# Optimization experiments

Hardware: AMD Instinct MI355X
Metric: run time of the kernel (lower is better)

The kernel has to match this reference:

```python
import jax, jax.numpy as jnp
import numpy as np

N_HEADS = 4
N_HIDDEN = 64  # out_features // n_heads
NEG_SLOPE = 0.2


def setup_inputs() -> dict:
    key = jax.random.key(0)
    k1, k2, k3, k4, k5 = jax.random.split(key, 5)
    B, N, F_IN, F_OUT = 1, 4096, 128, 256
    h = jax.random.normal(k1, (B, N, F_IN), dtype=jnp.float32)
    adj_mat = jax.random.uniform(k2, (N, N, 1), dtype=jnp.float32)
    W_proj = jax.random.normal(k3, (F_IN, N_HEADS * N_HIDDEN), dtype=jnp.float32) / np.sqrt(F_IN)
    W_proj_attn = jax.random.normal(k4, (F_IN, N_HEADS * N_HIDDEN // 2), dtype=jnp.float32) / np.sqrt(F_IN)
    w_attn = jax.random.normal(k5, (N_HIDDEN,), dtype=jnp.float32) / np.sqrt(N_HIDDEN)
    return {"h": h, "adj_mat": adj_mat, "W_proj": W_proj, "W_proj_attn": W_proj_attn, "w_attn": w_attn}


def reference(h, adj_mat, W_proj, W_proj_attn, w_attn):
    B, N, _ = h.shape
    H, D = N_HEADS, N_HIDDEN
    half = D // 2
    # value projection: (B, N, H, D)
    g = (h @ W_proj).reshape(B, N, H, D)
    # attention-feature projection: (B, N, H, D//2)
    ga = (h @ W_proj_attn).reshape(B, N, H, half)
    # attn(cat([ga_i, ga_j])) decomposes linearly: e_ij = <w_l, ga_i> + <w_r, ga_j>
    # (identical math to the torch repeat/cat/Linear, without the NxNxD tensor)
    el = jnp.einsum('bnhk,k->bnh', ga, w_attn[:half])   # dest node i term
    er = jnp.einsum('bnhk,k->bnh', ga, w_attn[half:])   # source node j term
    e = jax.nn.leaky_relu(el[:, :, None, :] + er[:, None, :, :], NEG_SLOPE)  # (B, N, N, H)
    mask = adj_mat >= 0.5  # (N, N, 1) broadcasts over (B, N, N, H)
    e = jnp.where(mask, e, -jnp.inf)
    a = jax.nn.softmax(e, axis=2)  # softmax over source nodes j
    # dropout is identity in eval mode
    out = jnp.einsum('bijh,bjhf->bihf', a, g)  # (B, N, H, D)
    return out.reshape(B, N, H * D)  # is_concat=True
```

## Files before the change

kernel.cpp:

```cpp
#include <hip/hip_runtime.h>
#include <hip/hip_bf16.h>

typedef __bf16 bf16_t;
typedef __bf16 bf16x4 __attribute__((ext_vector_type(4)));
typedef __bf16 bf16x8 __attribute__((ext_vector_type(8)));
typedef float floatx4 __attribute__((ext_vector_type(4)));

#define N_NODES 4096
#define F_IN 128
#define NUM_HEADS 4
#define D_HID 64
#define F_OUT 256
#define NEG_SLOPE 0.2f

__global__ __launch_bounds__(384) void proj_kernel(
    const float* __restrict__ hmat, const float* __restrict__ Wp,
    const float* __restrict__ Wa, const float* __restrict__ wattn,
    bf16_t* __restrict__ GB, float* __restrict__ el,
    float* __restrict__ E1r, float* __restrict__ E2r)
{
    __shared__ float hl[4][F_IN];
    const int t = threadIdx.x;
    const int j0 = blockIdx.x * 4;

    if (t < 128) {
        const int jl = t >> 5, m0 = (t & 31) * 4;
        *reinterpret_cast<float4*>(&hl[jl][m0]) =
            *reinterpret_cast<const float4*>(&hmat[(size_t)(j0 + jl) * F_IN + m0]);
    }
    __syncthreads();

    float acc[4] = {0.f, 0.f, 0.f, 0.f};

    const float* wptr;
    int stride;
    if (t < 256) { wptr = Wp + t;         stride = 256; }
    else         { wptr = Wa + (t - 256); stride = 128; }

    for (int m = 0; m < F_IN; m += 4) {
        const float w0 = wptr[(size_t)(m + 0) * stride];
        const float w1 = wptr[(size_t)(m + 1) * stride];
        const float w2 = wptr[(size_t)(m + 2) * stride];
        const float w3 = wptr[(size_t)(m + 3) * stride];
#pragma unroll
        for (int jl = 0; jl < 4; ++jl) {
            const float4 hv = *reinterpret_cast<const float4*>(&hl[jl][m]);
            acc[jl] = fmaf(hv.w, w3, fmaf(hv.z, w2, fmaf(hv.y, w1, fmaf(hv.x, w0, acc[jl]))));
        }
    }

    if (t < 256) {
        const int h = t >> 6, f = t & 63;
        bf16x4 o;
#pragma unroll
        for (int q = 0; q < 4; ++q) o[q] = (bf16_t)acc[q];
        const size_t base = ((((size_t)h * 128 + (j0 >> 5)) * 4 + (f >> 4)) * 64
                             + (f & 15) + 16 * ((j0 >> 3) & 3)) * 8 + (j0 & 7);
        *reinterpret_cast<bf16x4*>(&GB[base]) = o;
    } else {
        const int ta = t - 256;
        const int ha = ta >> 5, k = ta & 31;
        const float wl = wattn[k], wr = wattn[32 + k];
#pragma unroll
        for (int jl = 0; jl < 4; ++jl) {
            float vl = acc[jl] * wl;
            float vr = acc[jl] * wr;
#pragma unroll
            for (int s = 16; s >= 1; s >>= 1) {
                vl += __shfl_xor(vl, s, 64);
                vr += __shfl_xor(vr, s, 64);
            }
            if (k == 0) {
                el[ha * N_NODES + j0 + jl]  = vl;
                E1r[ha * N_NODES + j0 + jl] = __expf(vr);
                E2r[ha * N_NODES + j0 + jl] = __expf(NEG_SLOPE * vr);
            }
        }
    }
}

__global__ __launch_bounds__(1024, 4) void attn_kernel(
    const float* __restrict__ adj, const bf16_t* __restrict__ GB,
    const float* __restrict__ el, const float* __restrict__ E1r,
    const float* __restrict__ E2r,
    float* __restrict__ numout, float* __restrict__ den_g,
    int njc, int ntiles)
{
    __shared__ bf16_t P_s[2][NUM_HEADS * 64 * 64];
    __shared__ bf16_t GB_s[2][32 * 512];

    const int tid = threadIdx.x;
    const int i0  = blockIdx.x * 64;
    const int jc  = blockIdx.y;
    const int jT0 = jc * ntiles * 64;

    const int pi   = tid >> 4;
    const int pj4  = (tid & 15) << 2;
    const int glog = pj4 >> 3;
    const int goff = pj4 & 7;
    const int psw  = ((glog ^ (pi & 7)) << 3) + goff;

    const int wave = tid >> 6;
    const int hh   = wave >> 2;
    const int mt   = wave & 3;
    const int lane = tid & 63;
    const int m    = lane & 15;
    const int quad = lane >> 4;

    float E1i[NUM_HEADS], E2i[NUM_HEADS], Ti[NUM_HEADS];
#pragma unroll
    for (int h = 0; h < NUM_HEADS; ++h) {
        const float e = el[h * N_NODES + i0 + pi];
        E1i[h] = __expf(e);
        E2i[h] = __expf(NEG_SLOPE * e);
        Ti[h]  = __expf(-e);
    }

    const float* adjp = adj + (size_t)(i0 + pi) * N_NODES + pj4;

    const int s0 = wave * 2, s1 = s0 + 1;
    const int s0h = (s0 >> 2) & 3, s0f = s0 & 3, s0j = s0 >> 4;
    const int s1h = (s1 >> 2) & 3, s1f = s1 & 3, s1j = s1 >> 4;

    floatx4 acc0 = {0.f, 0.f, 0.f, 0.f};
    floatx4 acc1 = acc0, acc2 = acc0, acc3 = acc0, accd = acc0;
    bf16x8 ones;
#pragma unroll
    for (int q = 0; q < 8; ++q) ones[q] = (bf16_t)1.0f;

    auto do_mfma = [&](int b) {
#pragma unroll
        for (int kt = 0; kt < 2; ++kt) {
            const int gphys = (((kt * 4 + quad) ^ (m & 7)) << 3);
            const bf16x8 af = *reinterpret_cast<const bf16x8*>(
                &P_s[b][(hh * 64 + mt * 16 + m) * 64 + gphys]);
            accd = __builtin_amdgcn_mfma_f32_16x16x32_bf16(af, ones, accd, 0, 0, 0);
            const int bb = (kt * 16 + hh * 4) * 512 + lane * 8;
            const bf16x8 b0 = *reinterpret_cast<const bf16x8*>(&GB_s[b][bb]);
            const bf16x8 b1 = *reinterpret_cast<const bf16x8*>(&GB_s[b][bb + 512]);
            const bf16x8 b2 = *reinterpret_cast<const bf16x8*>(&GB_s[b][bb + 1024]);
            const bf16x8 b3 = *reinterpret_cast<const bf16x8*>(&GB_s[b][bb + 1536]);
            acc0 = __builtin_amdgcn_mfma_f32_16x16x32_bf16(af, b0, acc0, 0, 0, 0);
            acc1 = __builtin_amdgcn_mfma_f32_16x16x32_bf16(af, b1, acc1, 0, 0, 0);
            acc2 = __builtin_amdgcn_mfma_f32_16x16x32_bf16(af, b2, acc2, 0, 0, 0);
            acc3 = __builtin_amdgcn_mfma_f32_16x16x32_bf16(af, b3, acc3, 0, 0, 0);
        }
    };

    const int jb32 = jT0 >> 5;
    float4 adjv = *reinterpret_cast<const float4*>(adjp + jT0);
    float4 gbv0 = *reinterpret_cast<const float4*>(GB + ((size_t)(s0h * 128 + jb32 + s0j) * 4 + s0f) * 512 + lane * 8);
    float4 gbv1 = *reinterpret_cast<const float4*>(GB + ((size_t)(s1h * 128 + jb32 + s1j) * 4 + s1f) * 512 + lane * 8);

    int buf = 0;
    for (int k = 0; k < ntiles; ++k) {
        const int jT = jT0 + k * 64;
        *reinterpret_cast<float4*>(&GB_s[buf][s0 * 512 + lane * 8]) = gbv0;
        *reinterpret_cast<float4*>(&GB_s[buf][s1 * 512 + lane * 8]) = gbv1;

        float4 adjn, gbn0, gbn1;
        if (k + 1 < ntiles) {
            const int jbn = (jT + 64) >> 5;
            adjn = *reinterpret_cast<const float4*>(adjp + jT + 64);
            gbn0 = *reinterpret_cast<const float4*>(GB + ((size_t)(s0h * 128 + jbn + s0j) * 4 + s0f) * 512 + lane * 8);
            gbn1 = *reinterpret_cast<const float4*>(GB + ((size_t)(s1h * 128 + jbn + s1j) * 4 + s1f) * 512 + lane * 8);
        }

        const bool k0 = adjv.x >= 0.5f, k1 = adjv.y >= 0.5f,
                   k2 = adjv.z >= 0.5f, k3 = adjv.w >= 0.5f;
#pragma unroll
        for (int h = 0; h < NUM_HEADS; ++h) {
            const float4 a1 = *reinterpret_cast<const float4*>(E1r + h * N_NODES + jT + pj4);
            const float4 a2 = *reinterpret_cast<const float4*>(E2r + h * N_NODES + jT + pj4);
            const float p0 = (a1.x > Ti[h]) ? E1i[h] * a1.x : E2i[h] * a2.x;
            const float p1 = (a1.y > Ti[h]) ? E1i[h] * a1.y : E2i[h] * a2.y;
            const float p2 = (a1.z > Ti[h]) ? E1i[h] * a1.z : E2i[h] * a2.z;
            const float p3 = (a1.w > Ti[h]) ? E1i[h] * a1.w : E2i[h] * a2.w;
            bf16x4 pv;
            pv[0] = (bf16_t)(k0 ? p0 : 0.f);
            pv[1] = (bf16_t)(k1 ? p1 : 0.f);
            pv[2] = (bf16_t)(k2 ? p2 : 0.f);
            pv[3] = (bf16_t)(k3 ? p3 : 0.f);
            *reinterpret_cast<bf16x4*>(&P_s[buf][(h * 64 + pi) * 64 + psw]) = pv;
        }

        if (k > 0) do_mfma(buf ^ 1);

        __syncthreads();

        if (k + 1 < ntiles) { adjv = adjn; gbv0 = gbn0; gbv1 = gbn1; }
        buf ^= 1;
    }
    do_mfma(buf ^ 1);

    const int ibase = i0 + mt * 16 + quad * 4;
    if (njc == 1) {
#pragma unroll
        for (int r = 0; r < 4; ++r) {
            const float rd = 1.0f / accd[r];
            float* dst = numout + (size_t)(ibase + r) * F_OUT + hh * D_HID + m;
            dst[0]  = acc0[r] * rd;
            dst[16] = acc1[r] * rd;
            dst[32] = acc2[r] * rd;
            dst[48] = acc3[r] * rd;
        }
    } else {
        float* nrow = numout + (size_t)jc * ((size_t)N_NODES * F_OUT);
#pragma unroll
        for (int r = 0; r < 4; ++r) {
            float* dst = nrow + (size_t)(ibase + r) * F_OUT + hh * D_HID + m;
            dst[0]  = acc0[r];
            dst[16] = acc1[r];
            dst[32] = acc2[r];
            dst[48] = acc3[r];
        }
        if (m == 0) {
#pragma unroll
            for (int r = 0; r < 4; ++r)
                den_g[((size_t)jc * N_NODES + ibase + r) * NUM_HEADS + hh] = accd[r];
        }
    }
}

__global__ __launch_bounds__(256) void reduce_kernel(
    const float* __restrict__ num, const float* __restrict__ den,
    float* __restrict__ out, int njc)
{
    const int idx = blockIdx.x * 256 + threadIdx.x;
    const int i  = idx >> 8;
    const int c  = idx & 255;
    const int hh = c >> 6;
    float n = 0.f, d = 0.f;
    for (int jc = 0; jc < njc; ++jc) {
        n += num[(size_t)jc * ((size_t)N_NODES * F_OUT) + idx];
        d += den[((size_t)jc * N_NODES + i) * NUM_HEADS + hh];
    }
    out[idx] = n / d;
}

extern "C" void kernel_launch(void* const* d_in, const int* in_sizes, int n_in,
                              void* d_out, int out_size, void* d_ws, size_t ws_size,
                              hipStream_t stream)
{
    const float* hmat = (const float*)d_in[0];
    const float* adj  = (const float*)d_in[1];
    const float* Wp   = (const float*)d_in[2];
    const float* Wa   = (const float*)d_in[3];
    const float* watt = (const float*)d_in[4];
    float* out = (float*)d_out;

    char* ws = (char*)d_ws;
    bf16_t* GB  = (bf16_t*)ws;
    float*  el  = (float*)(ws + (2ull << 20));
    float*  E1r = (float*)(ws + (2ull << 20) + (64ull << 10));
    float*  E2r = (float*)(ws + (2ull << 20) + (128ull << 10));
    const size_t baseoff = (2ull << 20) + (192ull << 10);

    const size_t num_bytes = (size_t)N_NODES * F_OUT * 4;
    const size_t den_bytes = (size_t)N_NODES * NUM_HEADS * 4;
    const int njc = (ws_size >= baseoff + 4 * (num_bytes + den_bytes)) ? 4 : 2;

    float* num = (float*)(ws + baseoff);
    float* den = (float*)(ws + baseoff + (size_t)njc * num_bytes);

    proj_kernel<<<1024, 384, 0, stream>>>(hmat, Wp, Wa, watt, GB, el, E1r, E2r);
    attn_kernel<<<dim3(64, njc), 1024, 0, stream>>>(adj, GB, el, E1r, E2r,
                                                    num, den, njc, (N_NODES / njc) / 64);
    reduce_kernel<<<(N_NODES * F_OUT) / 256, 256, 0, stream>>>(num, den, out, njc);
}
```

Measured before the change: 166.4 us.

## Shrink attention tiles to 16 rows and build P fragments in registers

The attention kernel now uses 256-thread blocks covering 16 destination rows instead of 1024 threads covering 64 rows, which quadruples the grid. Each wave computes its softmax-numerator A fragment directly in registers from adjacency staged in LDS, and reads GB B-fragments straight from global memory instead of staging them in shared memory. This removes the P and GB LDS round trips and should raise occupancy. In exchange, the GB and E1/E2 vectors are re-read four times as often from global or L2, since each block now shares them over fewer rows.

```diff
diff --git a/kernel.cpp b/kernel.cpp
--- a/kernel.cpp
+++ b/kernel.cpp
@@ -79,48 +79,34 @@
     }
 }
 
-__global__ __launch_bounds__(1024, 4) void attn_kernel(
+__global__ __launch_bounds__(256, 4) void attn_kernel(
     const float* __restrict__ adj, const bf16_t* __restrict__ GB,
     const float* __restrict__ el, const float* __restrict__ E1r,
     const float* __restrict__ E2r,
     float* __restrict__ numout, float* __restrict__ den_g,
     int njc, int ntiles)
 {
-    __shared__ bf16_t P_s[2][NUM_HEADS * 64 * 64];
-    __shared__ bf16_t GB_s[2][32 * 512];
+    __shared__ float adj_s[2][16 * 68];
 
     const int tid = threadIdx.x;
-    const int i0  = blockIdx.x * 64;
+    const int i0  = blockIdx.x * 16;
     const int jc  = blockIdx.y;
     const int jT0 = jc * ntiles * 64;
 
-    const int pi   = tid >> 4;
-    const int pj4  = (tid & 15) << 2;
-    const int glog = pj4 >> 3;
-    const int goff = pj4 & 7;
-    const int psw  = ((glog ^ (pi & 7)) << 3) + goff;
-
-    const int wave = tid >> 6;
-    const int hh   = wave >> 2;
-    const int mt   = wave & 3;
+    const int r = tid >> 4;
+    const int c = tid & 15;
+
+    const int hh   = tid >> 6;
     const int lane = tid & 63;
     const int m    = lane & 15;
     const int quad = lane >> 4;
 
-    float E1i[NUM_HEADS], E2i[NUM_HEADS], Ti[NUM_HEADS];
-#pragma unroll
-    for (int h = 0; h < NUM_HEADS; ++h) {
-        const float e = el[h * N_NODES + i0 + pi];
-        E1i[h] = __expf(e);
-        E2i[h] = __expf(NEG_SLOPE * e);
-        Ti[h]  = __expf(-e);
-    }
-
-    const float* adjp = adj + (size_t)(i0 + pi) * N_NODES + pj4;
-
-    const int s0 = wave * 2, s1 = s0 + 1;
-    const int s0h = (s0 >> 2) & 3, s0f = s0 & 3, s0j = s0 >> 4;
-    const int s1h = (s1 >> 2) & 3, s1f = s1 & 3, s1j = s1 >> 4;
+    const float eli = el[hh * N_NODES + i0 + m];
+    const float E1i = __expf(eli);
+    const float E2i = __expf(NEG_SLOPE * eli);
+    const float Ti  = __expf(-eli);
+
+    const float* adjp = adj + (size_t)(i0 + r) * N_NODES + c * 4;
 
     floatx4 acc0 = {0.f, 0.f, 0.f, 0.f};
     floatx4 acc1 = acc0, acc2 = acc0, acc3 = acc0, accd = acc0;
@@ -128,96 +114,86 @@
 #pragma unroll
     for (int q = 0; q < 8; ++q) ones[q] = (bf16_t)1.0f;
 
-    auto do_mfma = [&](int b) {
+    float4 adjv = *reinterpret_cast<const float4*>(adjp + jT0);
+    *reinterpret_cast<float4*>(&adj_s[0][r * 68 + c * 4]) = adjv;
+    if (ntiles > 1)
+        adjv = *reinterpret_cast<const float4*>(adjp + jT0 + 64);
+    __syncthreads();
+
+    for (int k = 0; k < ntiles; ++k) {
+        const int buf = k & 1;
+        const int jT  = jT0 + k * 64;
+
+        if (k + 1 < ntiles) {
+            *reinterpret_cast<float4*>(&adj_s[buf ^ 1][r * 68 + c * 4]) = adjv;
+            if (k + 2 < ntiles)
+                adjv = *reinterpret_cast<const float4*>(adjp + jT + 128);
+        }
+
+        const float*  E1p = E1r + hh * N_NODES + jT + quad * 8;
+        const float*  E2p = E2r + hh * N_NODES + jT + quad * 8;
+        const bf16_t* gbb = GB + (size_t)(hh * 128 + (jT >> 5)) * 2048 + lane * 8;
+
 #pragma unroll
         for (int kt = 0; kt < 2; ++kt) {
-            const int gphys = (((kt * 4 + quad) ^ (m & 7)) << 3);
-            const bf16x8 af = *reinterpret_cast<const bf16x8*>(
-                &P_s[b][(hh * 64 + mt * 16 + m) * 64 + gphys]);
+            const float4 e1a = *reinterpret_cast<const float4*>(E1p + kt * 32);
+            const float4 e1b = *reinterpret_cast<const float4*>(E1p + kt * 32 + 4);
+            const float4 e2a = *reinterpret_cast<const float4*>(E2p + kt * 32);
+            const float4 e2b = *reinterpret_cast<const float4*>(E2p + kt * 32 + 4);
+            const float4 aa  = *reinterpret_cast<const float4*>(
+                &adj_s[buf][m * 68 + kt * 32 + quad * 8]);
+            const float4 ab  = *reinterpret_cast<const float4*>(
+                &adj_s[buf][m * 68 + kt * 32 + quad * 8 + 4]);
+
+            bf16x8 af;
+            af[0] = (aa.x >= 0.5f) ? (bf16_t)((e1a.x > Ti) ? E1i * e1a.x : E2i * e2a.x) : (bf16_t)0.f;
+            af[1] = (aa.y >= 0.5f) ? (bf16_t)((e1a.y > Ti) ? E1i * e1a.y : E2i * e2a.y) : (bf16_t)0.f;
+            af[2] = (aa.z >= 0.5f) ? (bf16_t)((e1a.z > Ti) ? E1i * e1a.z : E2i * e2a.z) : (bf16_t)0.f;
+            af[3] = (aa.w >= 0.5f) ? (bf16_t)((e1a.w > Ti) ? E1i * e1a.w : E2i * e2a.w) : (bf16_t)0.f;
+            af[4] = (ab.x >= 0.5f) ? (bf16_t)((e1b.x > Ti) ? E1i * e1b.x : E2i * e2b.x) : (bf16_t)0.f;
+            af[5] = (ab.y >= 0.5f) ? (bf16_t)((e1b.y > Ti) ? E1i * e1b.y : E2i * e2b.y) : (bf16_t)0.f;
+            af[6] = (ab.z >= 0.5f) ? (bf16_t)((e1b.z > Ti) ? E1i * e1b.z : E2i * e2b.z) : (bf16_t)0.f;
+            af[7] = (ab.w >= 0.5f) ? (bf16_t)((e1b.w > Ti) ? E1i * e1b.w : E2i * e2b.w) : (bf16_t)0.f;
+
+            const bf16x8 b0 = *reinterpret_cast<const bf16x8*>(gbb + kt * 2048);
+            const bf16x8 b1 = *reinterpret_cast<const bf16x8*>(gbb + kt * 2048 + 512);
+            const bf16x8 b2 = *reinterpret_cast<const bf16x8*>(gbb + kt * 2048 + 1024);
+            const bf16x8 b3 = *reinterpret_cast<const bf16x8*>(gbb + kt * 2048 + 1536);
+
             accd = __builtin_amdgcn_mfma_f32_16x16x32_bf16(af, ones, accd, 0, 0, 0);
-            const int bb = (kt * 16 + hh * 4) * 512 + lane * 8;
-            const bf16x8 b0 = *reinterpret_cast<const bf16x8*>(&GB_s[b][bb]);
-            const bf16x8 b1 = *reinterpret_cast<const bf16x8*>(&GB_s[b][bb + 512]);
-            const bf16x8 b2 = *reinterpret_cast<const bf16x8*>(&GB_s[b][bb + 1024]);
-            const bf16x8 b3 = *reinterpret_cast<const bf16x8*>(&GB_s[b][bb + 1536]);
             acc0 = __builtin_amdgcn_mfma_f32_16x16x32_bf16(af, b0, acc0, 0, 0, 0);
             acc1 = __builtin_amdgcn_mfma_f32_16x16x32_bf16(af, b1, acc1, 0, 0, 0);
             acc2 = __builtin_amdgcn_mfma_f32_16x16x32_bf16(af, b2, acc2, 0, 0, 0);
             acc3 = __builtin_amdgcn_mfma_f32_16x16x32_bf16(af, b3, acc3, 0, 0, 0);
         }
-    };
-
-    const int jb32 = jT0 >> 5;
-    float4 adjv = *reinterpret_cast<const float4*>(adjp + jT0);
-    float4 gbv0 = *reinterpret_cast<const float4*>(GB + ((size_t)(s0h * 128 + jb32 + s0j) * 4 + s0f) * 512 + lane * 8);
-    float4 gbv1 = *reinterpret_cast<const float4*>(GB + ((size_t)(s1h * 128 + jb32 + s1j) * 4 + s1f) * 512 + lane * 8);
-
-    int buf = 0;
-    for (int k = 0; k < ntiles; ++k) {
-        const int jT = jT0 + k * 64;
-        *reinterpret_cast<float4*>(&GB_s[buf][s0 * 512 + lane * 8]) = gbv0;
-        *reinterpret_cast<float4*>(&GB_s[buf][s1 * 512 + lane * 8]) = gbv1;
-
-        float4 adjn, gbn0, gbn1;
-        if (k + 1 < ntiles) {
-            const int jbn = (jT + 64) >> 5;
-            adjn = *reinterpret_cast<const float4*>(adjp + jT + 64);
-            gbn0 = *reinterpret_cast<const float4*>(GB + ((size_t)(s0h * 128 + jbn + s0j) * 4 + s0f) * 512 + lane * 8);
-            gbn1 = *reinterpret_cast<const float4*>(GB + ((size_t)(s1h * 128 + jbn + s1j) * 4 + s1f) * 512 + lane * 8);
-        }
-
-        const bool k0 = adjv.x >= 0.5f, k1 = adjv.y >= 0.5f,
-                   k2 = adjv.z >= 0.5f, k3 = adjv.w >= 0.5f;
-#pragma unroll
-        for (int h = 0; h < NUM_HEADS; ++h) {
-            const float4 a1 = *reinterpret_cast<const float4*>(E1r + h * N_NODES + jT + pj4);
-            const float4 a2 = *reinterpret_cast<const float4*>(E2r + h * N_NODES + jT + pj4);
-            const float p0 = (a1.x > Ti[h]) ? E1i[h] * a1.x : E2i[h] * a2.x;
-            const float p1 = (a1.y > Ti[h]) ? E1i[h] * a1.y : E2i[h] * a2.y;
-            const float p2 = (a1.z > Ti[h]) ? E1i[h] * a1.z : E2i[h] * a2.z;
-            const float p3 = (a1.w > Ti[h]) ? E1i[h] * a1.w : E2i[h] * a2.w;
-            bf16x4 pv;
-            pv[0] = (bf16_t)(k0 ? p0 : 0.f);
-            pv[1] = (bf16_t)(k1 ? p1 : 0.f);
-            pv[2] = (bf16_t)(k2 ? p2 : 0.f);
-            pv[3] = (bf16_t)(k3 ? p3 : 0.f);
-            *reinterpret_cast<bf16x4*>(&P_s[buf][(h * 64 + pi) * 64 + psw]) = pv;
-        }
-
-        if (k > 0) do_mfma(buf ^ 1);
-
         __syncthreads();
-
-        if (k + 1 < ntiles) { adjv = adjn; gbv0 = gbn0; gbv1 = gbn1; }
-        buf ^= 1;
-    }
-    do_mfma(buf ^ 1);
-
-    const int ibase = i0 + mt * 16 + quad * 4;
+    }
+
+    const int ibase = i0 + quad * 4;
     if (njc == 1) {
 #pragma unroll
-        for (int r = 0; r < 4; ++r) {
-            const float rd = 1.0f / accd[r];
-            float* dst = numout + (size_t)(ibase + r) * F_OUT + hh * D_HID + m;
-            dst[0]  = acc0[r] * rd;
-            dst[16] = acc1[r] * rd;
-            dst[32] = acc2[r] * rd;
-            dst[48] = acc3[r] * rd;
+        for (int rr = 0; rr < 4; ++rr) {
+            const float rd = 1.0f / accd[rr];
+            float* dst = numout + (size_t)(ibase + rr) * F_OUT + hh * D_HID + m;
+            dst[0]  = acc0[rr] * rd;
+            dst[16] = acc1[rr] * rd;
+            dst[32] = acc2[rr] * rd;
+            dst[48] = acc3[rr] * rd;
         }
     } else {
         float* nrow = numout + (size_t)jc * ((size_t)N_NODES * F_OUT);
 #pragma unroll
-        for (int r = 0; r < 4; ++r) {
-            float* dst = nrow + (size_t)(ibase + r) * F_OUT + hh * D_HID + m;
-            dst[0]  = acc0[r];
-            dst[16] = acc1[r];
-            dst[32] = acc2[r];
-            dst[48] = acc3[r];
+        for (int rr = 0; rr < 4; ++rr) {
+            float* dst = nrow + (size_t)(ibase + rr) * F_OUT + hh * D_HID + m;
+            dst[0]  = acc0[rr];
+            dst[16] = acc1[rr];
+            dst[32] = acc2[rr];
+            dst[48] = acc3[rr];
         }
         if (m == 0) {
 #pragma unroll
-            for (int r = 0; r < 4; ++r)
-                den_g[((size_t)jc * N_NODES + ibase + r) * NUM_HEADS + hh] = accd[r];
+            for (int rr = 0; rr < 4; ++rr)
+                den_g[((size_t)jc * N_NODES + ibase + rr) * NUM_HEADS + hh] = accd[rr];
         }
     }
 }
@@ -264,7 +240,7 @@
     float* den = (float*)(ws + baseoff + (size_t)njc * num_bytes);
 
     proj_kernel<<<1024, 384, 0, stream>>>(hmat, Wp, Wa, watt, GB, el, E1r, E2r);
-    attn_kernel<<<dim3(64, njc), 1024, 0, stream>>>(adj, GB, el, E1r, E2r,
+    attn_kernel<<<dim3(256, njc), 256, 0, stream>>>(adj, GB, el, E1r, E2r,
                                                     num, den, njc, (N_NODES / njc) / 64);
     reduce_kernel<<<(N_NODES * F_OUT) / 256, 256, 0, stream>>>(num, den, out, njc);
 }
```

New measurement: 163.4 us. Within noise of the previous version (-1.8%).
